# Kernel tuning notes

Hardware: AMD Instinct MI355X
Metric: run time of the kernel (lower is better)

## Reference

```python
import jax, jax.numpy as jnp
import numpy as np


def setup_inputs() -> dict:
    key = jax.random.key(0)
    k1, k2 = jax.random.split(key)
    B, T, F, S, C = 16, 1024, 8, 128, 256
    e_src = jax.random.normal(k1, (B, T, F, C), dtype=jnp.float32)
    d_src = jax.random.randint(k2, (B, S), 0, 16, dtype=jnp.int64)
    return {"e_src": e_src, "d_src": d_src}


def reference(e_src, d_src):
    # Ragged per-phone mean pooling (the nested python loop in FastSpeech2Pros.forward):
    # e_src: [B, T_mel, F, C]; d_src: [B, S] frame durations per phone.
    # For b in range(B//2): chunk e_src[b] along T by durations, mean over (time, freq),
    # zeros for empty chunks -> agg [B//2, S, C].
    B, T, F, C = e_src.shape
    Bh = B // 2
    S = d_src.shape[1]
    e = e_src[:Bh]                      # [Bh, T, F, C]
    d = d_src[:Bh].astype(jnp.int32)    # [Bh, S]

    # frame t belongs to phone i iff cumsum(d)[i-1] <= t < cumsum(d)[i]
    cum = jnp.cumsum(d, axis=1)                                   # [Bh, S]
    t = jnp.arange(T, dtype=jnp.int32)
    seg = jax.vmap(lambda c: jnp.searchsorted(c, t, side='right'))(cum)  # [Bh, T]
    seg = jnp.minimum(seg, S)           # frames beyond total duration -> overflow bucket S

    frame_sum = e.sum(axis=2)           # [Bh, T, C] (sum over freq dim)
    sums = jax.vmap(
        lambda fs, s: jax.ops.segment_sum(fs, s, num_segments=S + 1)
    )(frame_sum, seg)[:, :S]            # [Bh, S, C]

    counts = (d * F).astype(e.dtype)    # elements per ragged chunk = dur * F
    agg = jnp.where(counts[..., None] > 0,
                    sums / jnp.maximum(counts, 1.0)[..., None],
                    jnp.zeros((), e.dtype))
    return agg
```

## Files before the change

### kernel.cpp

```cpp
#include <hip/hip_runtime.h>

#define TT 1024
#define SS 128
#define FF 8
#define CC 256
#define BH 8

__global__ __launch_bounds__(256) void fused_kernel(const float* __restrict__ e,
                                                    const int* __restrict__ dsrc,
                                                    float* __restrict__ out) {
    int s = blockIdx.x;
    int b = blockIdx.y;
    int tid = threadIdx.x;
    int c4 = tid & 63;
    int q  = tid >> 6;

    __shared__ int cumbuf[SS];
    if (tid < SS) cumbuf[tid] = dsrc[b * SS + tid];
    __syncthreads();
    #pragma unroll
    for (int off = 1; off < SS; off <<= 1) {
        int v = 0;
        if (tid < SS && tid >= off) v = cumbuf[tid - off];
        __syncthreads();
        if (tid < SS) cumbuf[tid] += v;
        __syncthreads();
    }

    int end   = cumbuf[s];
    int start = (s == 0) ? 0 : cumbuf[s - 1];
    int dc    = dsrc[b * SS + s];
    if (start > TT) start = TT;
    if (end   > TT) end   = TT;
    int K = (end - start) * FF;

    const float4* e4 = (const float4*)(e + (size_t)(b * TT + start) * (FF * CC));

    float ax = 0.f, ay = 0.f, az = 0.f, aw = 0.f;
    int k = q;
    for (; k + 12 < K; k += 16) {
        float4 v0 = e4[(size_t)(k     ) * 64 + c4];
        float4 v1 = e4[(size_t)(k +  4) * 64 + c4];
        float4 v2 = e4[(size_t)(k +  8) * 64 + c4];
        float4 v3 = e4[(size_t)(k + 12) * 64 + c4];
        ax += v0.x + v1.x + v2.x + v3.x;
        ay += v0.y + v1.y + v2.y + v3.y;
        az += v0.z + v1.z + v2.z + v3.z;
        aw += v0.w + v1.w + v2.w + v3.w;
    }
    for (; k < K; k += 4) {
        float4 v = e4[(size_t)k * 64 + c4];
        ax += v.x; ay += v.y; az += v.z; aw += v.w;
    }

    __shared__ float4 red[256];
    red[tid] = make_float4(ax, ay, az, aw);
    __syncthreads();

    if (q == 0) {
        float4 r0 = red[tid];
        float4 r1 = red[tid + 64];
        float4 r2 = red[tid + 128];
        float4 r3 = red[tid + 192];
        float inv = (dc > 0) ? (1.0f / (float)(dc * FF)) : 0.0f;
        float4 r;
        r.x = (r0.x + r1.x + r2.x + r3.x) * inv;
        r.y = (r0.y + r1.y + r2.y + r3.y) * inv;
        r.z = (r0.z + r1.z + r2.z + r3.z) * inv;
        r.w = (r0.w + r1.w + r2.w + r3.w) * inv;
        ((float4*)out)[(size_t)(b * SS + s) * 64 + c4] = r;
    }
}

extern "C" void kernel_launch(void* const* d_in, const int* in_sizes, int n_in,
                              void* d_out, int out_size, void* d_ws, size_t ws_size,
                              hipStream_t stream) {
    const float* e   = (const float*)d_in[0];
    const int*   d   = (const int*)d_in[1];
    float*       out = (float*)d_out;

    fused_kernel<<<dim3(SS, BH), 256, 0, stream>>>(e, d, out);
}
```

Measured before the change: 174.8 us.

## Parallelize pooling over fixed time chunks with atomic segment accumulation

Replaces the one-block-per-phone layout with one block per fixed four-frame chunk of time. Each block binary-searches the segment of every frame and flushes partial sums into the output with atomicAdd, after a separate kernel zeroes the output. The goal is even load balancing, since the old per-phone blocks had ragged and often tiny work. The cost is an extra launch, a binary search per frame, scalar instead of float4 loads, and atomic traffic.

```diff
diff --git a/kernel.cpp b/kernel.cpp
--- a/kernel.cpp
+++ b/kernel.cpp
@@ -5,15 +5,19 @@
 #define FF 8
 #define CC 256
 #define BH 8
+#define CHUNK_T 4
+#define NCHUNK (TT / CHUNK_T)
 
-__global__ __launch_bounds__(256) void fused_kernel(const float* __restrict__ e,
-                                                    const int* __restrict__ dsrc,
-                                                    float* __restrict__ out) {
-    int s = blockIdx.x;
-    int b = blockIdx.y;
-    int tid = threadIdx.x;
-    int c4 = tid & 63;
-    int q  = tid >> 6;
+__global__ __launch_bounds__(256) void zero_out(float4* __restrict__ out) {
+    out[blockIdx.x * 256 + threadIdx.x] = make_float4(0.f, 0.f, 0.f, 0.f);
+}
+
+__global__ __launch_bounds__(256) void agg_atomic(const float* __restrict__ e,
+                                                  const int* __restrict__ dsrc,
+                                                  float* __restrict__ out) {
+    int chunk = blockIdx.x;
+    int b     = blockIdx.y;
+    int tid   = threadIdx.x;
 
     __shared__ int cumbuf[SS];
     if (tid < SS) cumbuf[tid] = dsrc[b * SS + tid];
@@ -27,48 +31,44 @@
         __syncthreads();
     }
 
-    int end   = cumbuf[s];
-    int start = (s == 0) ? 0 : cumbuf[s - 1];
-    int dc    = dsrc[b * SS + s];
-    if (start > TT) start = TT;
-    if (end   > TT) end   = TT;
-    int K = (end - start) * FF;
+    int t0 = chunk * CHUNK_T;
+    const float* ep = e + ((size_t)b * TT + t0) * (FF * CC) + tid;
 
-    const float4* e4 = (const float4*)(e + (size_t)(b * TT + start) * (FF * CC));
+    float acc = 0.f;
+    int cur_seg = -1;
 
-    float ax = 0.f, ay = 0.f, az = 0.f, aw = 0.f;
-    int k = q;
-    for (; k + 12 < K; k += 16) {
-        float4 v0 = e4[(size_t)(k     ) * 64 + c4];
-        float4 v1 = e4[(size_t)(k +  4) * 64 + c4];
-        float4 v2 = e4[(size_t)(k +  8) * 64 + c4];
-        float4 v3 = e4[(size_t)(k + 12) * 64 + c4];
-        ax += v0.x + v1.x + v2.x + v3.x;
-        ay += v0.y + v1.y + v2.y + v3.y;
-        az += v0.z + v1.z + v2.z + v3.z;
-        aw += v0.w + v1.w + v2.w + v3.w;
+    #pragma unroll
+    for (int i = 0; i < CHUNK_T; i++) {
+        int t = t0 + i;
+        int lo = 0, hi = SS;
+        while (lo < hi) {
+            int mid = (lo + hi) >> 1;
+            if (cumbuf[mid] <= t) lo = mid + 1; else hi = mid;
+        }
+        int seg = lo;
+
+        if (seg != cur_seg) {
+            if (cur_seg >= 0 && cur_seg < SS) {
+                int dlo = (cur_seg == 0) ? 0 : cumbuf[cur_seg - 1];
+                int dc  = cumbuf[cur_seg] - dlo;
+                float inv = 1.0f / (float)(dc * FF);
+                atomicAdd(&out[((size_t)b * SS + cur_seg) * CC + tid], acc * inv);
+            }
+            acc = 0.f;
+            cur_seg = seg;
+        }
+        if (seg < SS) {
+            float v = 0.f;
+            #pragma unroll
+            for (int f = 0; f < FF; f++) v += ep[(size_t)(i * FF + f) * CC];
+            acc += v;
+        }
     }
-    for (; k < K; k += 4) {
-        float4 v = e4[(size_t)k * 64 + c4];
-        ax += v.x; ay += v.y; az += v.z; aw += v.w;
-    }
-
-    __shared__ float4 red[256];
-    red[tid] = make_float4(ax, ay, az, aw);
-    __syncthreads();
-
-    if (q == 0) {
-        float4 r0 = red[tid];
-        float4 r1 = red[tid + 64];
-        float4 r2 = red[tid + 128];
-        float4 r3 = red[tid + 192];
-        float inv = (dc > 0) ? (1.0f / (float)(dc * FF)) : 0.0f;
-        float4 r;
-        r.x = (r0.x + r1.x + r2.x + r3.x) * inv;
-        r.y = (r0.y + r1.y + r2.y + r3.y) * inv;
-        r.z = (r0.z + r1.z + r2.z + r3.z) * inv;
-        r.w = (r0.w + r1.w + r2.w + r3.w) * inv;
-        ((float4*)out)[(size_t)(b * SS + s) * 64 + c4] = r;
+    if (cur_seg >= 0 && cur_seg < SS) {
+        int dlo = (cur_seg == 0) ? 0 : cumbuf[cur_seg - 1];
+        int dc  = cumbuf[cur_seg] - dlo;
+        float inv = 1.0f / (float)(dc * FF);
+        atomicAdd(&out[((size_t)b * SS + cur_seg) * CC + tid], acc * inv);
     }
 }
 
@@ -79,5 +79,6 @@
     const int*   d   = (const int*)d_in[1];
     float*       out = (float*)d_out;
 
-    fused_kernel<<<dim3(SS, BH), 256, 0, stream>>>(e, d, out);
+    zero_out<<<256, 256, 0, stream>>>((float4*)out);
+    agg_atomic<<<dim3(NCHUNK, BH), 256, 0, stream>>>(e, d, out);
 }
```

New measurement: 175.0 us. No clear change (+0.1%).
